# Optimization experiments

Hardware: AMD Instinct MI355X
Metric: run time of the kernel (lower is better)

The kernel has to match this reference:

```python
import jax, jax.numpy as jnp
import numpy as np

H = 16  # num_heads
D = 1024  # hidden_size

def setup_inputs() -> dict:
    key = jax.random.key(0)
    ks = jax.random.split(key, 9)
    s = 1.0 / np.sqrt(D).astype(np.float32)
    return {
        'x':  jax.random.normal(ks[0], (2, 2048, D), dtype=jnp.float32),
        'wq': jax.random.normal(ks[1], (D, D), dtype=jnp.float32) * s,
        'bq': jax.random.normal(ks[2], (D,), dtype=jnp.float32) * s,
        'wk': jax.random.normal(ks[3], (D, D), dtype=jnp.float32) * s,
        'bk': jax.random.normal(ks[4], (D,), dtype=jnp.float32) * s,
        'wv': jax.random.normal(ks[5], (D, D), dtype=jnp.float32) * s,
        'bv': jax.random.normal(ks[6], (D,), dtype=jnp.float32) * s,
        'wo': jax.random.normal(ks[7], (D, D), dtype=jnp.float32) * s,
        'bo': jax.random.normal(ks[8], (D,), dtype=jnp.float32) * s,
    }

def _split_heads(t):
    # [b, s, (h d)] -> [b, h, s, d]
    b, s, _ = t.shape
    return t.reshape(b, s, H, D // H).transpose(0, 2, 1, 3)

def reference(x, wq, bq, wk, bk, wv, bv, wo, bo):
    q = _split_heads(x @ wq + bq)  # [b, h, s, d]
    k = _split_heads(x @ wk + bk)
    v = _split_heads(x @ wv + bv)
    scale = 1.0 / jnp.sqrt(jnp.asarray(q.shape[-1], q.dtype))
    attn = jnp.einsum('bhqd,bhkd->bhqk', q, k) * scale
    attn = jax.nn.softmax(attn, axis=-1)
    o = jnp.einsum('bhqk,bhkd->bhqd', attn, v)
    b, h, s, d = o.shape
    o = o.transpose(0, 2, 1, 3).reshape(b, s, h * d)  # concat heads
    return o @ wo + bo
```

## Files before the change

### kernel.cpp

```cpp
#include <hip/hip_runtime.h>
#include <stdint.h>
#include <stddef.h>


typedef __bf16 bf16_t;
typedef __bf16 bf16x8 __attribute__((ext_vector_type(8)));
typedef __bf16 bf16x4 __attribute__((ext_vector_type(4)));
typedef __bf16 bf16x2 __attribute__((ext_vector_type(2)));
typedef float  f32x4  __attribute__((ext_vector_type(4)));
typedef float  f32x8  __attribute__((ext_vector_type(8)));
typedef float  f32x16 __attribute__((ext_vector_type(16)));
typedef uint32_t u32x4 __attribute__((ext_vector_type(4)));

static constexpr float kQScale = 0.18033688011112042f;

__device__ __forceinline__ void gload_lds16(const bf16_t* g, bf16_t* l) {
  __builtin_amdgcn_global_load_lds((__attribute__((address_space(1))) void*)(void*)g,
                                   (__attribute__((address_space(3))) void*)l, 16, 0, 0);
}

__device__ __forceinline__ uint32_t pk_bf16(float lo, float hi) {
  bf16x2 v; v[0] = (bf16_t)lo; v[1] = (bf16_t)hi;
  return __builtin_bit_cast(uint32_t, v);
}

__global__ __launch_bounds__(256) void prep_k(
    const float* __restrict__ x, bf16_t* __restrict__ xb,
    const float* __restrict__ wq, const float* __restrict__ wk,
    const float* __restrict__ wv, const float* __restrict__ wo,
    bf16_t* __restrict__ wqkvT, bf16_t* __restrict__ woT) {
  __shared__ float t[64][65];
  const int z = blockIdx.z;
  if (z == 4) {
    const int blk = blockIdx.y * 16 + blockIdx.x;
#pragma unroll
    for (int c = 0; c < 16; ++c) {
      const int i = c * 65536 + blk * 256 + threadIdx.x;
      float4 v = ((const float4*)x)[i];
      bf16x4 o;
      o[0] = (bf16_t)v.x; o[1] = (bf16_t)v.y; o[2] = (bf16_t)v.z; o[3] = (bf16_t)v.w;
      ((bf16x4*)xb)[i] = o;
    }
    return;
  }
  const float* src = z == 0 ? wq : z == 1 ? wk : z == 2 ? wv : wo;
  bf16_t* dst = z < 3 ? wqkvT + (size_t)z * 1024 * 1024 : woT;
  int n0 = blockIdx.x * 64, k0 = blockIdx.y * 64;
  int c = threadIdx.x & 63, r4 = threadIdx.x >> 6;
#pragma unroll
  for (int i = 0; i < 16; ++i) {
    int r = r4 + i * 4;
    t[r][c] = src[(size_t)(k0 + r) * 1024 + (n0 + c)];
  }
  __syncthreads();
#pragma unroll
  for (int i = 0; i < 16; ++i) {
    int r = r4 + i * 4;
    dst[(size_t)(n0 + r) * 1024 + (k0 + c)] = (bf16_t)t[c][r];
  }
}

__global__ __launch_bounds__(256) void gemm_qkv_k(
    const bf16_t* __restrict__ A, const bf16_t* __restrict__ Bw,
    bf16_t* __restrict__ Qb, bf16_t* __restrict__ Kb, bf16_t* __restrict__ Vt,
    const float* __restrict__ bq, const float* __restrict__ bk, const float* __restrict__ bv) {
  __shared__ alignas(16) bf16_t As[128 * 32];
  __shared__ alignas(16) bf16_t Bs[128 * 32];
  const int tid = threadIdx.x;
  const int lane = tid & 63;
  const int w = tid >> 6, wr = w >> 1, wc = w & 1;
  const int brow = blockIdx.y * 128, bcol = blockIdx.x * 128;
  const int l15 = lane & 15, ko = (lane >> 4) * 8;

  f32x4 acc[4][4] = {};
  const bf16_t* Ab = A + (size_t)brow * 1024;
  const bf16_t* Bb = Bw + (size_t)bcol * 1024;

  const int e0 = tid * 8;
  const int r0 = e0 >> 5, c0 = e0 & 31;

  for (int k0 = 0; k0 < 1024; k0 += 32) {
    gload_lds16(Ab + (size_t)r0 * 1024 + k0 + c0, &As[e0]);
    gload_lds16(Ab + (size_t)(r0 + 64) * 1024 + k0 + c0, &As[e0 + 2048]);
    gload_lds16(Bb + (size_t)r0 * 1024 + k0 + c0, &Bs[e0]);
    gload_lds16(Bb + (size_t)(r0 + 64) * 1024 + k0 + c0, &Bs[e0 + 2048]);
    __syncthreads();
    bf16x8 af[4], bfg[4];
#pragma unroll
    for (int i = 0; i < 4; ++i)
      af[i] = *(const bf16x8*)&As[(wr * 64 + i * 16 + l15) * 32 + ko];
#pragma unroll
    for (int i = 0; i < 4; ++i)
      bfg[i] = *(const bf16x8*)&Bs[(wc * 64 + i * 16 + l15) * 32 + ko];
#pragma unroll
    for (int i = 0; i < 4; ++i)
#pragma unroll
      for (int j = 0; j < 4; ++j)
        acc[i][j] = __builtin_amdgcn_mfma_f32_16x16x32_bf16(af[i], bfg[j], acc[i][j], 0, 0, 0);
    __syncthreads();
  }

  const int mat = bcol >> 10;
#pragma unroll
  for (int i = 0; i < 4; ++i) {
    const int gm0 = brow + wr * 64 + i * 16 + ((lane >> 4) << 2);
    const int b = gm0 >> 11, s0 = gm0 & 2047;
#pragma unroll
    for (int j = 0; j < 4; ++j) {
      const int gn = bcol + wc * 64 + j * 16 + l15;
      const int col = gn & 1023;
      const int h = col >> 6, dd = col & 63;
      if (mat == 2) {
        const float bsv = bv[col];
        bf16x4 pk;
#pragma unroll
        for (int r = 0; r < 4; ++r) pk[r] = (bf16_t)(acc[i][j][r] + bsv);
        *(bf16x4*)&Vt[(((size_t)b * 16 + h) * 64 + dd) * 2048 + s0] = pk;
      } else {
        bf16_t* dst = mat == 0 ? Qb : Kb;
        const float bsv = (mat == 0 ? bq : bk)[col];
        const float scl = mat == 0 ? kQScale : 1.0f;
#pragma unroll
        for (int r = 0; r < 4; ++r)
          dst[((((size_t)b * 16 + h) * 2048 + (s0 + r)) * 64 + dd)] = (bf16_t)((acc[i][j][r] + bsv) * scl);
      }
    }
  }
}

__global__ __launch_bounds__(256) void gemm_out_k(
    const bf16_t* __restrict__ A, const bf16_t* __restrict__ Bw,
    float* __restrict__ outF, const float* __restrict__ bo) {
  __shared__ alignas(16) bf16_t As[128 * 32];
  __shared__ alignas(16) bf16_t Bs[64 * 32];
  const int tid = threadIdx.x;
  const int lane = tid & 63;
  const int w = tid >> 6;
  const int brow = blockIdx.y * 128, bcol = blockIdx.x * 64;
  const int l15 = lane & 15, ko = (lane >> 4) * 8;

  f32x4 acc[2][4] = {};
  const bf16_t* Ab = A + (size_t)brow * 1024;
  const bf16_t* Bb = Bw + (size_t)bcol * 1024;

  const int e0 = tid * 8;
  const int r0 = e0 >> 5, c0 = e0 & 31;

  for (int k0 = 0; k0 < 1024; k0 += 32) {
    gload_lds16(Ab + (size_t)r0 * 1024 + k0 + c0, &As[e0]);
    gload_lds16(Ab + (size_t)(r0 + 64) * 1024 + k0 + c0, &As[e0 + 2048]);
    gload_lds16(Bb + (size_t)r0 * 1024 + k0 + c0, &Bs[e0]);
    __syncthreads();
    bf16x8 af[2], bfg[4];
#pragma unroll
    for (int i = 0; i < 2; ++i)
      af[i] = *(const bf16x8*)&As[(w * 32 + i * 16 + l15) * 32 + ko];
#pragma unroll
    for (int j = 0; j < 4; ++j)
      bfg[j] = *(const bf16x8*)&Bs[(j * 16 + l15) * 32 + ko];
#pragma unroll
    for (int i = 0; i < 2; ++i)
#pragma unroll
      for (int j = 0; j < 4; ++j)
        acc[i][j] = __builtin_amdgcn_mfma_f32_16x16x32_bf16(af[i], bfg[j], acc[i][j], 0, 0, 0);
    __syncthreads();
  }

#pragma unroll
  for (int i = 0; i < 2; ++i) {
    const int gm0 = brow + w * 32 + i * 16 + ((lane >> 4) << 2);
#pragma unroll
    for (int j = 0; j < 4; ++j) {
      const int gn = bcol + j * 16 + l15;
      const float bsv = bo[gn];
#pragma unroll
      for (int r = 0; r < 4; ++r)
        outF[(size_t)(gm0 + r) * 1024 + gn] = acc[i][j][r] + bsv;
    }
  }
}

__global__ __launch_bounds__(512, 2) void attn_k(
    const bf16_t* __restrict__ Qb, const bf16_t* __restrict__ Kb,
    const bf16_t* __restrict__ Vt, bf16_t* __restrict__ O) {
  __shared__ alignas(16) bf16_t Ksm[2][2][4096];
  __shared__ alignas(16) bf16_t Vsm[2][2][4096];
  const int tid = threadIdx.x, lane = tid & 63, w = tid >> 6;
  const int l31 = lane & 31, hi = lane >> 5;
  const int qsub = w & 3, half = w >> 2;
  const int work = (blockIdx.x & 7) * 64 + (blockIdx.x >> 3);
  const int bh = work >> 4;
  const int q0 = (work & 15) * 128 + qsub * 32;

  const bf16_t* Qp = Qb + ((size_t)bh * 2048 + q0) * 64;

  const int chunk0 = qsub * 64 + lane;
  const int srow = chunk0 >> 3;
  const int swzc = (chunk0 & 7) ^ (srow & 7);
  const char* srcK0 = (const char*)(Kb + ((size_t)bh * 2048 + half * 1024) * 64) + srow * 128 + swzc * 16;
  const char* srcK1 = srcK0 + 32 * 128;
  const char* srcV0 = (const char*)(Vt + (size_t)bh * 64 * 2048 + half * 1024) + srow * 4096 + swzc * 16;
  const char* srcV1 = srcV0 + 32 * 4096;

  auto stage = [&](int buf) {
    bf16_t* kb = &Ksm[half][buf][qsub * 512];
    bf16_t* vb = &Vsm[half][buf][qsub * 512];
    gload_lds16((const bf16_t*)srcK0, kb);
    gload_lds16((const bf16_t*)srcK1, kb + 2048);
    gload_lds16((const bf16_t*)srcV0, vb);
    gload_lds16((const bf16_t*)srcV1, vb + 2048);
    srcK0 += 8192; srcK1 += 8192;
    srcV0 += 128;  srcV1 += 128;
  };

  const int xorv = l31 & 7;
  const bf16_t* kcb[4];
#pragma unroll
  for (int j = 0; j < 4; ++j) {
    const int co = ((j * 2 + hi) ^ xorv) * 8;
    kcb[j] = &Ksm[half][0][l31 * 64 + co];
  }
  const bf16_t* vptr[8];
#pragma unroll
  for (int c = 0; c < 8; ++c)
    vptr[c] = &Vsm[half][0][l31 * 64 + ((c ^ xorv) << 3) + 4 * hi];

  bf16x8 qf[4];
#pragma unroll
  for (int ds = 0; ds < 4; ++ds)
    qf[ds] = *(const bf16x8*)&Qp[(size_t)l31 * 64 + ds * 16 + hi * 8];

  f32x16 o0 = {}, o1 = {};
  float mx = -1e30f, li = 0.0f;

  auto tile_body = [&](int buf) {
    const int bo = buf * 4096;
    bf16x8 kf0[4], kf1[4];
#pragma unroll
    for (int ds = 0; ds < 4; ++ds) {
      kf0[ds] = *(const bf16x8*)(kcb[ds] + bo);
      kf1[ds] = *(const bf16x8*)(kcb[ds] + bo + 2048);
    }
    f32x16 s0 = {}, s1 = {};
    __builtin_amdgcn_s_setprio(1);
#pragma unroll
    for (int ds = 0; ds < 4; ++ds)
      s0 = __builtin_amdgcn_mfma_f32_32x32x16_bf16(kf0[ds], qf[ds], s0, 0, 0, 0);
#pragma unroll
    for (int ds = 0; ds < 4; ++ds)
      s1 = __builtin_amdgcn_mfma_f32_32x32x16_bf16(kf1[ds], qf[ds], s1, 0, 0, 0);
    __builtin_amdgcn_s_setprio(0);

    f32x16 mm = __builtin_elementwise_max(s0, s1);
    f32x8 ma = __builtin_shufflevector(mm, mm, 0, 1, 2, 3, 4, 5, 6, 7);
    f32x8 mb = __builtin_shufflevector(mm, mm, 8, 9, 10, 11, 12, 13, 14, 15);
    f32x8 m8 = __builtin_elementwise_max(ma, mb);
    f32x4 m4 = __builtin_elementwise_max(
        __builtin_shufflevector(m8, m8, 0, 1, 2, 3),
        __builtin_shufflevector(m8, m8, 4, 5, 6, 7));
    float tmax = fmaxf(fmaxf(m4[0], m4[1]), fmaxf(m4[2], m4[3]));
    tmax = fmaxf(tmax, __shfl_xor(tmax, 32));

    if (__any(tmax > mx + 8.0f)) {
      const float mn = fmaxf(mx, tmax);
      const float corr = __builtin_amdgcn_exp2f(mx - mn);
      mx = mn;
      li *= corr;
      o0 *= corr;
      o1 *= corr;
    }

    s0 -= mx;
    s1 -= mx;
#pragma unroll
    for (int r = 0; r < 16; ++r) {
      s0[r] = __builtin_amdgcn_exp2f(s0[r]);
      s1[r] = __builtin_amdgcn_exp2f(s1[r]);
    }
    f32x16 sv = s0 + s1;
    f32x8 sv8 = __builtin_shufflevector(sv, sv, 0, 1, 2, 3, 4, 5, 6, 7) +
                __builtin_shufflevector(sv, sv, 8, 9, 10, 11, 12, 13, 14, 15);
    f32x4 sv4 = __builtin_shufflevector(sv8, sv8, 0, 1, 2, 3) +
                __builtin_shufflevector(sv8, sv8, 4, 5, 6, 7);
    float rs = (sv4[0] + sv4[1]) + (sv4[2] + sv4[3]);
    rs += __shfl_xor(rs, 32);
    li += rs;

    uint32_t pw0[8], pw1[8];
#pragma unroll
    for (int g = 0; g < 4; ++g) {
      pw0[g * 2 + 0] = pk_bf16(s0[4 * g + 0], s0[4 * g + 1]);
      pw0[g * 2 + 1] = pk_bf16(s0[4 * g + 2], s0[4 * g + 3]);
      pw1[g * 2 + 0] = pk_bf16(s1[4 * g + 0], s1[4 * g + 1]);
      pw1[g * 2 + 1] = pk_bf16(s1[4 * g + 2], s1[4 * g + 3]);
    }

#pragma unroll
    for (int st = 0; st < 2; ++st) {
      uint32_t (&pw)[8] = st ? pw1 : pw0;
#pragma unroll
      for (int ks = 0; ks < 2; ++ks) {
        const bf16_t* pA = vptr[4 * st + 2 * ks] + bo;
        const bf16_t* pB = vptr[4 * st + 2 * ks + 1] + bo;
        const bf16x4 a0 = *(const bf16x4*)pA;
        const bf16x4 a1 = *(const bf16x4*)pB;
        const bf16x4 b0 = *(const bf16x4*)(pA + 2048);
        const bf16x4 b1 = *(const bf16x4*)(pB + 2048);
        u32x4 fq;
        fq[0] = pw[4 * ks + 0];
        fq[1] = pw[4 * ks + 1];
        fq[2] = pw[4 * ks + 2];
        fq[3] = pw[4 * ks + 3];
        const bf16x8 pf = __builtin_bit_cast(bf16x8, fq);
        const bf16x8 v0 = __builtin_shufflevector(a0, a1, 0, 1, 2, 3, 4, 5, 6, 7);
        const bf16x8 v1 = __builtin_shufflevector(b0, b1, 0, 1, 2, 3, 4, 5, 6, 7);
        __builtin_amdgcn_s_setprio(1);
        o0 = __builtin_amdgcn_mfma_f32_32x32x16_bf16(v0, pf, o0, 0, 0, 0);
        o1 = __builtin_amdgcn_mfma_f32_32x32x16_bf16(v1, pf, o1, 0, 0, 0);
        __builtin_amdgcn_s_setprio(0);
      }
    }
  };

  stage(0);
  __syncthreads();
#pragma unroll 1
  for (int t = 0; t < 16; t += 2) {
    stage(1);
    tile_body(0);
    __syncthreads();
    if (t + 2 < 16) stage(0);
    tile_body(1);
    if (t + 2 < 16) __syncthreads();
  }

  __syncthreads();
  float* cmb_o = (float*)&Ksm[0][0][0];
  float* cmb_m = (float*)&Vsm[0][0][0];
  float* cmb_l = cmb_m + 256;
  if (half) {
    cmb_m[qsub * 64 + lane] = mx;
    cmb_l[qsub * 64 + lane] = li;
#pragma unroll
    for (int r = 0; r < 16; ++r) {
      cmb_o[(qsub * 32 + r) * 64 + lane] = o0[r];
      cmb_o[(qsub * 32 + 16 + r) * 64 + lane] = o1[r];
    }
  }
  __syncthreads();
  if (!half) {
    const float mb = cmb_m[qsub * 64 + lane];
    const float lb = cmb_l[qsub * 64 + lane];
    const float M = fmaxf(mx, mb);
    const float ca = __builtin_amdgcn_exp2f(mx - M);
    const float cb = __builtin_amdgcn_exp2f(mb - M);
    const float L = li * ca + lb * cb;
    const float inv = 1.0f / L;
    const float fa = ca * inv, fb = cb * inv;
    const int b = bh >> 4, h = bh & 15;
    const size_t row = (size_t)b * 2048 + q0 + l31;
#pragma unroll
    for (int g = 0; g < 4; ++g) {
      bf16x4 p0, p1;
#pragma unroll
      for (int r = 0; r < 4; ++r) {
        p0[r] = (bf16_t)(o0[4 * g + r] * fa + cmb_o[(qsub * 32 + 4 * g + r) * 64 + lane] * fb);
        p1[r] = (bf16_t)(o1[4 * g + r] * fa + cmb_o[(qsub * 32 + 16 + 4 * g + r) * 64 + lane] * fb);
      }
      *(bf16x4*)&O[row * 1024 + h * 64 + 0  + g * 8 + hi * 4] = p0;
      *(bf16x4*)&O[row * 1024 + h * 64 + 32 + g * 8 + hi * 4] = p1;
    }
  }
}

extern "C" void kernel_launch(void* const* d_in, const int* in_sizes, int n_in,
                              void* d_out, int out_size, void* d_ws, size_t ws_size,
                              hipStream_t stream) {
  const float* x  = (const float*)d_in[0];
  const float* wq = (const float*)d_in[1];
  const float* bq = (const float*)d_in[2];
  const float* wk = (const float*)d_in[3];
  const float* bk = (const float*)d_in[4];
  const float* wv = (const float*)d_in[5];
  const float* bv = (const float*)d_in[6];
  const float* wo = (const float*)d_in[7];
  const float* bo = (const float*)d_in[8];
  float* out = (float*)d_out;

  if (ws_size < ((size_t)48 << 20)) return;
  char* ws = (char*)d_ws;
  bf16_t* xb  = (bf16_t*)(ws);
  bf16_t* wT  = (bf16_t*)(ws + ((size_t)8 << 20));
  bf16_t* woT = wT + (size_t)3072 * 1024;
  bf16_t* Qb  = (bf16_t*)(ws + ((size_t)16 << 20));
  bf16_t* Kb  = (bf16_t*)(ws + ((size_t)24 << 20));
  bf16_t* Vt  = (bf16_t*)(ws + ((size_t)32 << 20));
  bf16_t* O   = xb;

  prep_k<<<dim3(16, 16, 5), 256, 0, stream>>>(x, xb, wq, wk, wv, wo, wT, woT);
  gemm_qkv_k<<<dim3(24, 32), 256, 0, stream>>>(xb, wT, Qb, Kb, Vt, bq, bk, bv);
  attn_k<<<512, 512, 0, stream>>>(Qb, Kb, Vt, O);
  gemm_out_k<<<dim3(16, 32), 256, 0, stream>>>(O, woT, out, bo);
}
```

Baseline: 122.0 us.

## Process two 32-row query blocks per wave in attention to reuse K/V fragments

Each attention wave now handles 64 query rows (two 32-row sub-blocks) instead of 32, so every K and V fragment read from LDS feeds twice as many MFMAs. The grid is halved to 256 blocks and the launch-bounds occupancy hint is dropped. The split-KV combine step now runs twice through shared memory. This is meant to cut LDS traffic and global K/V staging per query, at the cost of more registers, lower occupancy, and fewer blocks than CUs (256 CUs on MI355X means one block per CU).

```diff
diff --git a/kernel.cpp b/kernel.cpp
--- a/kernel.cpp
+++ b/kernel.cpp
@@ -180,7 +180,7 @@
   }
 }
 
-__global__ __launch_bounds__(512, 2) void attn_k(
+__global__ __launch_bounds__(512) void attn_k(
     const bf16_t* __restrict__ Qb, const bf16_t* __restrict__ Kb,
     const bf16_t* __restrict__ Vt, bf16_t* __restrict__ O) {
   __shared__ alignas(16) bf16_t Ksm[2][2][4096];
@@ -188,9 +188,9 @@
   const int tid = threadIdx.x, lane = tid & 63, w = tid >> 6;
   const int l31 = lane & 31, hi = lane >> 5;
   const int qsub = w & 3, half = w >> 2;
-  const int work = (blockIdx.x & 7) * 64 + (blockIdx.x >> 3);
-  const int bh = work >> 4;
-  const int q0 = (work & 15) * 128 + qsub * 32;
+  const int work = (blockIdx.x & 7) * 32 + (blockIdx.x >> 3);
+  const int bh = work >> 3;
+  const int q0 = (work & 7) * 256 + qsub * 64;
 
   const bf16_t* Qp = Qb + ((size_t)bh * 2048 + q0) * 64;
 
@@ -225,51 +225,35 @@
   for (int c = 0; c < 8; ++c)
     vptr[c] = &Vsm[half][0][l31 * 64 + ((c ^ xorv) << 3) + 4 * hi];
 
-  bf16x8 qf[4];
-#pragma unroll
-  for (int ds = 0; ds < 4; ++ds)
-    qf[ds] = *(const bf16x8*)&Qp[(size_t)l31 * 64 + ds * 16 + hi * 8];
-
-  f32x16 o0 = {}, o1 = {};
-  float mx = -1e30f, li = 0.0f;
-
-  auto tile_body = [&](int buf) {
-    const int bo = buf * 4096;
-    bf16x8 kf0[4], kf1[4];
-#pragma unroll
-    for (int ds = 0; ds < 4; ++ds) {
-      kf0[ds] = *(const bf16x8*)(kcb[ds] + bo);
-      kf1[ds] = *(const bf16x8*)(kcb[ds] + bo + 2048);
-    }
-    f32x16 s0 = {}, s1 = {};
-    __builtin_amdgcn_s_setprio(1);
+  bf16x8 qf[2][4];
+#pragma unroll
+  for (int qb = 0; qb < 2; ++qb)
 #pragma unroll
     for (int ds = 0; ds < 4; ++ds)
-      s0 = __builtin_amdgcn_mfma_f32_32x32x16_bf16(kf0[ds], qf[ds], s0, 0, 0, 0);
-#pragma unroll
-    for (int ds = 0; ds < 4; ++ds)
-      s1 = __builtin_amdgcn_mfma_f32_32x32x16_bf16(kf1[ds], qf[ds], s1, 0, 0, 0);
-    __builtin_amdgcn_s_setprio(0);
-
+      qf[qb][ds] = *(const bf16x8*)&Qp[(size_t)(qb * 32 + l31) * 64 + ds * 16 + hi * 8];
+
+  f32x16 oA0 = {}, oA1 = {}, oB0 = {}, oB1 = {};
+  float mxA = -1e30f, liA = 0.0f, mxB = -1e30f, liB = 0.0f;
+
+  auto softmax_pack = [&](f32x16& s0, f32x16& s1, float& mx, float& li,
+                          f32x16& oa, f32x16& ob, uint32_t* pw0, uint32_t* pw1) {
     f32x16 mm = __builtin_elementwise_max(s0, s1);
-    f32x8 ma = __builtin_shufflevector(mm, mm, 0, 1, 2, 3, 4, 5, 6, 7);
-    f32x8 mb = __builtin_shufflevector(mm, mm, 8, 9, 10, 11, 12, 13, 14, 15);
-    f32x8 m8 = __builtin_elementwise_max(ma, mb);
+    f32x8 m8 = __builtin_elementwise_max(
+        __builtin_shufflevector(mm, mm, 0, 1, 2, 3, 4, 5, 6, 7),
+        __builtin_shufflevector(mm, mm, 8, 9, 10, 11, 12, 13, 14, 15));
     f32x4 m4 = __builtin_elementwise_max(
         __builtin_shufflevector(m8, m8, 0, 1, 2, 3),
         __builtin_shufflevector(m8, m8, 4, 5, 6, 7));
     float tmax = fmaxf(fmaxf(m4[0], m4[1]), fmaxf(m4[2], m4[3]));
     tmax = fmaxf(tmax, __shfl_xor(tmax, 32));
-
     if (__any(tmax > mx + 8.0f)) {
       const float mn = fmaxf(mx, tmax);
       const float corr = __builtin_amdgcn_exp2f(mx - mn);
       mx = mn;
       li *= corr;
-      o0 *= corr;
-      o1 *= corr;
-    }
-
+      oa *= corr;
+      ob *= corr;
+    }
     s0 -= mx;
     s1 -= mx;
 #pragma unroll
@@ -285,8 +269,6 @@
     float rs = (sv4[0] + sv4[1]) + (sv4[2] + sv4[3]);
     rs += __shfl_xor(rs, 32);
     li += rs;
-
-    uint32_t pw0[8], pw1[8];
 #pragma unroll
     for (int g = 0; g < 4; ++g) {
       pw0[g * 2 + 0] = pk_bf16(s0[4 * g + 0], s0[4 * g + 1]);
@@ -294,10 +276,36 @@
       pw1[g * 2 + 0] = pk_bf16(s1[4 * g + 0], s1[4 * g + 1]);
       pw1[g * 2 + 1] = pk_bf16(s1[4 * g + 2], s1[4 * g + 3]);
     }
+  };
+
+  auto tile_body = [&](int buf) {
+    const int bo = buf * 4096;
+    bf16x8 kf0[4], kf1[4];
+#pragma unroll
+    for (int ds = 0; ds < 4; ++ds) {
+      kf0[ds] = *(const bf16x8*)(kcb[ds] + bo);
+      kf1[ds] = *(const bf16x8*)(kcb[ds] + bo + 2048);
+    }
+    f32x16 sA0 = {}, sA1 = {}, sB0 = {}, sB1 = {};
+    __builtin_amdgcn_s_setprio(1);
+#pragma unroll
+    for (int ds = 0; ds < 4; ++ds) {
+      sA0 = __builtin_amdgcn_mfma_f32_32x32x16_bf16(kf0[ds], qf[0][ds], sA0, 0, 0, 0);
+      sB0 = __builtin_amdgcn_mfma_f32_32x32x16_bf16(kf0[ds], qf[1][ds], sB0, 0, 0, 0);
+    }
+#pragma unroll
+    for (int ds = 0; ds < 4; ++ds) {
+      sA1 = __builtin_amdgcn_mfma_f32_32x32x16_bf16(kf1[ds], qf[0][ds], sA1, 0, 0, 0);
+      sB1 = __builtin_amdgcn_mfma_f32_32x32x16_bf16(kf1[ds], qf[1][ds], sB1, 0, 0, 0);
+    }
+    __builtin_amdgcn_s_setprio(0);
+
+    uint32_t pwA0[8], pwA1[8], pwB0[8], pwB1[8];
+    softmax_pack(sA0, sA1, mxA, liA, oA0, oA1, pwA0, pwA1);
+    softmax_pack(sB0, sB1, mxB, liB, oB0, oB1, pwB0, pwB1);
 
 #pragma unroll
     for (int st = 0; st < 2; ++st) {
-      uint32_t (&pw)[8] = st ? pw1 : pw0;
 #pragma unroll
       for (int ks = 0; ks < 2; ++ks) {
         const bf16_t* pA = vptr[4 * st + 2 * ks] + bo;
@@ -306,17 +314,22 @@
         const bf16x4 a1 = *(const bf16x4*)pB;
         const bf16x4 b0 = *(const bf16x4*)(pA + 2048);
         const bf16x4 b1 = *(const bf16x4*)(pB + 2048);
-        u32x4 fq;
-        fq[0] = pw[4 * ks + 0];
-        fq[1] = pw[4 * ks + 1];
-        fq[2] = pw[4 * ks + 2];
-        fq[3] = pw[4 * ks + 3];
-        const bf16x8 pf = __builtin_bit_cast(bf16x8, fq);
         const bf16x8 v0 = __builtin_shufflevector(a0, a1, 0, 1, 2, 3, 4, 5, 6, 7);
         const bf16x8 v1 = __builtin_shufflevector(b0, b1, 0, 1, 2, 3, 4, 5, 6, 7);
+        const uint32_t* pwA = st ? pwA1 : pwA0;
+        const uint32_t* pwB = st ? pwB1 : pwB0;
+        u32x4 fa, fb;
+        fa[0] = pwA[4 * ks + 0]; fa[1] = pwA[4 * ks + 1];
+        fa[2] = pwA[4 * ks + 2]; fa[3] = pwA[4 * ks + 3];
+        fb[0] = pwB[4 * ks + 0]; fb[1] = pwB[4 * ks + 1];
+        fb[2] = pwB[4 * ks + 2]; fb[3] = pwB[4 * ks + 3];
+        const bf16x8 pfA = __builtin_bit_cast(bf16x8, fa);
+        const bf16x8 pfB = __builtin_bit_cast(bf16x8, fb);
         __builtin_amdgcn_s_setprio(1);
-        o0 = __builtin_amdgcn_mfma_f32_32x32x16_bf16(v0, pf, o0, 0, 0, 0);
-        o1 = __builtin_amdgcn_mfma_f32_32x32x16_bf16(v1, pf, o1, 0, 0, 0);
+        oA0 = __builtin_amdgcn_mfma_f32_32x32x16_bf16(v0, pfA, oA0, 0, 0, 0);
+        oA1 = __builtin_amdgcn_mfma_f32_32x32x16_bf16(v1, pfA, oA1, 0, 0, 0);
+        oB0 = __builtin_amdgcn_mfma_f32_32x32x16_bf16(v0, pfB, oB0, 0, 0, 0);
+        oB1 = __builtin_amdgcn_mfma_f32_32x32x16_bf16(v1, pfB, oB1, 0, 0, 0);
         __builtin_amdgcn_s_setprio(0);
       }
     }
@@ -335,37 +348,70 @@
   }
 
   __syncthreads();
-  float* cmb_o = (float*)&Ksm[0][0][0];
-  float* cmb_m = (float*)&Vsm[0][0][0];
-  float* cmb_l = cmb_m + 256;
+  float* cmb_o  = (float*)&Ksm[0][0][0];
+  float* cmb_ml = (float*)&Vsm[0][0][0];
+  const int b = bh >> 4, h = bh & 15;
+
   if (half) {
-    cmb_m[qsub * 64 + lane] = mx;
-    cmb_l[qsub * 64 + lane] = li;
+    cmb_ml[((0 * 2 + 0) * 4 + qsub) * 64 + lane] = mxA;
+    cmb_ml[((0 * 2 + 1) * 4 + qsub) * 64 + lane] = liA;
+    cmb_ml[((1 * 2 + 0) * 4 + qsub) * 64 + lane] = mxB;
+    cmb_ml[((1 * 2 + 1) * 4 + qsub) * 64 + lane] = liB;
 #pragma unroll
     for (int r = 0; r < 16; ++r) {
-      cmb_o[(qsub * 32 + r) * 64 + lane] = o0[r];
-      cmb_o[(qsub * 32 + 16 + r) * 64 + lane] = o1[r];
+      cmb_o[(qsub * 32 + r) * 64 + lane] = oA0[r];
+      cmb_o[(qsub * 32 + 16 + r) * 64 + lane] = oA1[r];
     }
   }
   __syncthreads();
   if (!half) {
-    const float mb = cmb_m[qsub * 64 + lane];
-    const float lb = cmb_l[qsub * 64 + lane];
-    const float M = fmaxf(mx, mb);
-    const float ca = __builtin_amdgcn_exp2f(mx - M);
+    const float mb = cmb_ml[((0 * 2 + 0) * 4 + qsub) * 64 + lane];
+    const float lb = cmb_ml[((0 * 2 + 1) * 4 + qsub) * 64 + lane];
+    const float M = fmaxf(mxA, mb);
+    const float ca = __builtin_amdgcn_exp2f(mxA - M);
     const float cb = __builtin_amdgcn_exp2f(mb - M);
-    const float L = li * ca + lb * cb;
+    const float L = liA * ca + lb * cb;
     const float inv = 1.0f / L;
     const float fa = ca * inv, fb = cb * inv;
-    const int b = bh >> 4, h = bh & 15;
     const size_t row = (size_t)b * 2048 + q0 + l31;
 #pragma unroll
     for (int g = 0; g < 4; ++g) {
       bf16x4 p0, p1;
 #pragma unroll
       for (int r = 0; r < 4; ++r) {
-        p0[r] = (bf16_t)(o0[4 * g + r] * fa + cmb_o[(qsub * 32 + 4 * g + r) * 64 + lane] * fb);
-        p1[r] = (bf16_t)(o1[4 * g + r] * fa + cmb_o[(qsub * 32 + 16 + 4 * g + r) * 64 + lane] * fb);
+        p0[r] = (bf16_t)(oA0[4 * g + r] * fa + cmb_o[(qsub * 32 + 4 * g + r) * 64 + lane] * fb);
+        p1[r] = (bf16_t)(oA1[4 * g + r] * fa + cmb_o[(qsub * 32 + 16 + 4 * g + r) * 64 + lane] * fb);
+      }
+      *(bf16x4*)&O[row * 1024 + h * 64 + 0  + g * 8 + hi * 4] = p0;
+      *(bf16x4*)&O[row * 1024 + h * 64 + 32 + g * 8 + hi * 4] = p1;
+    }
+  }
+  __syncthreads();
+  if (half) {
+#pragma unroll
+    for (int r = 0; r < 16; ++r) {
+      cmb_o[(qsub * 32 + r) * 64 + lane] = oB0[r];
+      cmb_o[(qsub * 32 + 16 + r) * 64 + lane] = oB1[r];
+    }
+  }
+  __syncthreads();
+  if (!half) {
+    const float mb = cmb_ml[((1 * 2 + 0) * 4 + qsub) * 64 + lane];
+    const float lb = cmb_ml[((1 * 2 + 1) * 4 + qsub) * 64 + lane];
+    const float M = fmaxf(mxB, mb);
+    const float ca = __builtin_amdgcn_exp2f(mxB - M);
+    const float cb = __builtin_amdgcn_exp2f(mb - M);
+    const float L = liB * ca + lb * cb;
+    const float inv = 1.0f / L;
+    const float fa = ca * inv, fb = cb * inv;
+    const size_t row = (size_t)b * 2048 + q0 + 32 + l31;
+#pragma unroll
+    for (int g = 0; g < 4; ++g) {
+      bf16x4 p0, p1;
+#pragma unroll
+      for (int r = 0; r < 4; ++r) {
+        p0[r] = (bf16_t)(oB0[4 * g + r] * fa + cmb_o[(qsub * 32 + 4 * g + r) * 64 + lane] * fb);
+        p1[r] = (bf16_t)(oB1[4 * g + r] * fa + cmb_o[(qsub * 32 + 16 + 4 * g + r) * 64 + lane] * fb);
       }
       *(bf16x4*)&O[row * 1024 + h * 64 + 0  + g * 8 + hi * 4] = p0;
       *(bf16x4*)&O[row * 1024 + h * 64 + 32 + g * 8 + hi * 4] = p1;
@@ -399,6 +445,6 @@
 
   prep_k<<<dim3(16, 16, 5), 256, 0, stream>>>(x, xb, wq, wk, wv, wo, wT, woT);
   gemm_qkv_k<<<dim3(24, 32), 256, 0, stream>>>(xb, wT, Qb, Kb, Vt, bq, bk, bv);
-  attn_k<<<512, 512, 0, stream>>>(Qb, Kb, Vt, O);
+  attn_k<<<256, 512, 0, stream>>>(Qb, Kb, Vt, O);
   gemm_out_k<<<dim3(16, 32), 256, 0, stream>>>(O, woT, out, bo);
 }
```

New measurement: 116.7 us. 1.05x faster.
